# Kernel optimization log

Measured on AMD Instinct MI355X. Metric: run time of the kernel, lower is better.

Reference implementation:

```python
import jax, jax.numpy as jnp
import numpy as np

B, S, E, H, L = 32, 1024, 768, 64, 2  # batch, seq (<=1024 per bias buffer), embed, head hidden, labels
MASKED_BIAS = jnp.float32(-10000.0)


def setup_inputs() -> dict:
    key = jax.random.key(0)
    ks = jax.random.split(key, 12)
    s = 0.02  # init scale
    return {
        "hidden": jax.random.normal(ks[0], (B, S, E), dtype=jnp.float32),
        "attention_mask": jnp.ones((B, S), dtype=jnp.float32),
        # torch nn.Linear weights are [out, in]
        "Wk": jax.random.normal(ks[1], (E, E), dtype=jnp.float32) * s,
        "bk": jnp.zeros((E,), dtype=jnp.float32),
        "Wq": jax.random.normal(ks[2], (E, E), dtype=jnp.float32) * s,
        "bq": jnp.zeros((E,), dtype=jnp.float32),
        "Wv": jax.random.normal(ks[3], (E, E), dtype=jnp.float32) * s,
        "bv": jnp.zeros((E,), dtype=jnp.float32),
        "W1": jax.random.normal(ks[4], (H, E), dtype=jnp.float32) * s,
        "b1": jnp.zeros((H,), dtype=jnp.float32),
        "W2": jax.random.normal(ks[5], (L, H), dtype=jnp.float32) * s,
        "b2": jnp.zeros((L,), dtype=jnp.float32),
    }


def reference(hidden, attention_mask, Wk, bk, Wq, bq, Wv, bv, W1, b1, W2, b2):
    # Single-head causal attention, NO 1/sqrt(d) scaling (faithful to source).
    # Dropout layers run in eval mode -> identity.
    seq = hidden.shape[1]
    q = hidden @ Wq.T + bq            # [B,S,E]
    k = hidden @ Wk.T + bk            # [B,S,E]
    v = hidden @ Wv.T + bv            # [B,S,E] (v_drop is identity in eval)
    w = jnp.einsum('bqe,bke->bqk', q, k)  # [B,S,S]
    causal = jnp.tril(jnp.ones((seq, seq), dtype=bool))  # bias[:, ns-nd:ns, :ns] with nd==ns
    w = jnp.where(causal, w, MASKED_BIAS.astype(w.dtype))
    am = (1.0 - attention_mask)[:, None, :] * -10000.0    # [B,1,S]
    w = jax.nn.softmax(w + am, axis=-1)
    h = jnp.einsum('bqk,bke->bqe', w, v)  # [B,S,E]
    h = jax.nn.relu(h @ W1.T + b1)        # [B,S,64]
    return h @ W2.T + b2                  # [B,S,L]
```

## Files before the change

kernel.cpp:

```cpp
#include <hip/hip_runtime.h>
#include <hip/hip_bf16.h>
#include <cstdio>


typedef _Float16 f16;
typedef f16    f16x8 __attribute__((ext_vector_type(8)));
typedef f16    f16x4 __attribute__((ext_vector_type(4)));
typedef __bf16 bfx8  __attribute__((ext_vector_type(8)));
typedef float  f32x4 __attribute__((ext_vector_type(4)));

#define MFMA_F16(a,b,c)  __builtin_amdgcn_mfma_f32_16x16x32_f16((a),(b),(c),0,0,0)
#define MFMA_BF16(a,b,c) __builtin_amdgcn_mfma_f32_16x16x32_bf16((a),(b),(c),0,0,0)

static constexpr int LDT = 136;
static constexpr int LDT2 = 264;

__device__ __forceinline__ void gl_lds16(const void* g, void* l) {
    __builtin_amdgcn_global_load_lds(
        (const __attribute__((address_space(1))) void*)g,
        (__attribute__((address_space(3))) void*)l, 16, 0, 0);
}

__global__ __launch_bounds__(256) void cvt_f32_f16(
    const float* __restrict__ x, f16* __restrict__ y, int n)
{
    int base = (blockIdx.x * 256 + threadIdx.x) * 4;
    if (base >= n) return;
    f32x4 v = *(const f32x4*)(x + base);
    f16x4 o;
    #pragma unroll
    for (int e = 0; e < 4; ++e) o[e] = (f16)v[e];
    *(f16x4*)(y + base) = o;
}

__global__ __launch_bounds__(256) void cvt3_w(
    const float* __restrict__ Wq, const float* __restrict__ Wk, const float* __restrict__ Wv,
    f16* __restrict__ oq, f16* __restrict__ ok, f16* __restrict__ ov)
{
    const int z = blockIdx.y;
    const float* s = (z == 0) ? Wq : (z == 1) ? Wk : Wv;
    f16* d = (z == 0) ? oq : (z == 1) ? ok : ov;
    int base = (blockIdx.x * 256 + threadIdx.x) * 4;
    f32x4 v = *(const f32x4*)(s + base);
    f16x4 o;
    #pragma unroll
    for (int e = 0; e < 4; ++e) o[e] = (f16)v[e];
    *(f16x4*)(d + base) = o;
}

__global__ __launch_bounds__(1024, 4) void qkv_kernel(
    const f16* __restrict__ h16,
    const f16* __restrict__ wq, const f16* __restrict__ wk, const f16* __restrict__ wv,
    const float* __restrict__ bq, const float* __restrict__ bk, const float* __restrict__ bv,
    f16* __restrict__ q16, f16* __restrict__ k16, __bf16* __restrict__ vT)
{
    const int f = blockIdx.x;
    const int xcd = f & 7;
    const int j = f >> 3;
    const int nt = j % 3;
    const int z  = (j / 3) % 3;
    const int mi = j / 9;
    const int mt = xcd + 8 * mi;
    const int m0 = mt * 256, n0 = nt * 256;

    const f16* W = (z == 0) ? wq : (z == 1) ? wk : wv;
    const float* bias = (z == 0) ? bq : (z == 1) ? bk : bv;

    __shared__ alignas(16) char smem[67584];
    f16 (*S)[16384] = (f16 (*)[16384])smem;
    __bf16* Tb = (__bf16*)smem;

    const int t = threadIdx.x, lane = t & 63, wave = t >> 6;
    const int wm = (wave & 3) * 64, wn = (wave >> 2) * 64;
    const int quad = lane >> 4, l16 = lane & 15;

    const f16* gsrc[2];
    int ldst[2];
    #pragma unroll
    for (int u = 0; u < 2; ++u) {
        int c = wave * 2 + u;
        ldst[u] = c * 512;
        int row = (c < 16) ? (m0 + c * 16 + l16) : (n0 + (c - 16) * 16 + l16);
        const f16* base = (c < 16) ? h16 : W;
        gsrc[u] = base + (size_t)row * 768 + quad * 8;
    }

    f32x4 acc[4][4] = {};
    auto stage = [&](int k0, int buf) {
        #pragma unroll
        for (int u = 0; u < 2; ++u)
            gl_lds16(gsrc[u] + k0, &S[buf][ldst[u]]);
    };
    auto compute = [&](int buf) {
        f16x8 af[4], bg[4];
        #pragma unroll
        for (int i = 0; i < 4; ++i) {
            af[i] = *(const f16x8*)&S[buf][(wm / 16 + i) * 512 + quad * 128 + l16 * 8];
            bg[i] = *(const f16x8*)&S[buf][(16 + wn / 16 + i) * 512 + quad * 128 + l16 * 8];
        }
        #pragma unroll
        for (int i = 0; i < 4; ++i)
            #pragma unroll
            for (int jj = 0; jj < 4; ++jj)
                acc[i][jj] = MFMA_F16(af[i], bg[jj], acc[i][jj]);
    };

    stage(0, 0);
    int cur = 0;
    for (int k0 = 32; k0 < 768; k0 += 32) {
        __syncthreads();
        stage(k0, cur ^ 1);
        compute(cur);
        cur ^= 1;
    }
    __syncthreads();
    compute(cur);

    if (z < 2) {
        f16* out = z ? k16 : q16;
        #pragma unroll
        for (int jj = 0; jj < 4; ++jj) {
            int col = n0 + wn + jj * 16 + l16;
            float bb = bias[col];
            #pragma unroll
            for (int i = 0; i < 4; ++i)
                #pragma unroll
                for (int r = 0; r < 4; ++r) {
                    int row = m0 + wm + i * 16 + quad * 4 + r;
                    out[(size_t)row * 768 + col] = (f16)(acc[i][jj][r] + bb);
                }
        }
    } else {
        const int bofs = (m0 >> 10) * 768;
        const int s0 = m0 & 1023;
        #pragma unroll
        for (int half = 0; half < 2; ++half) {
            __syncthreads();
            if ((wn >> 7) == half) {
                int wnl = wn & 127;
                #pragma unroll
                for (int jj = 0; jj < 4; ++jj) {
                    int el = wnl + jj * 16 + l16;
                    float bb = bias[n0 + half * 128 + el];
                    #pragma unroll
                    for (int i = 0; i < 4; ++i)
                        #pragma unroll
                        for (int r = 0; r < 4; ++r) {
                            int sl = wm + i * 16 + quad * 4 + r;
                            Tb[el * LDT2 + sl] = (__bf16)(acc[i][jj][r] + bb);
                        }
                }
            }
            __syncthreads();
            const int ch = (t & 31) * 8;
            const int rbase = t >> 5;
            #pragma unroll
            for (int p = 0; p < 4; ++p) {
                int r2 = rbase + p * 32;
                bfx8 val = *(const bfx8*)&Tb[r2 * LDT2 + ch];
                *(bfx8*)&vT[(size_t)(bofs + n0 + half * 128 + r2) * 1024 + s0 + ch] = val;
            }
        }
    }
}

__global__ __launch_bounds__(512, 4) void logits_kernel(
    const f16* __restrict__ q16, const f16* __restrict__ k16,
    const float* __restrict__ amask, __bf16* __restrict__ pu, float* __restrict__ psum)
{
    const int f = blockIdx.x;
    const int xcd = f & 7;
    const int j = f >> 3;
    const int b = xcd + 8 * (j / 20);
    const int tile = j % 20;
    const int mt = (tile < 2) ? 0 : (tile < 6) ? 1 : (tile < 12) ? 2 : 3;
    const int nt = tile - ((mt == 0) ? 0 : (mt == 1) ? 2 : (mt == 2) ? 6 : 12);
    const int m0 = mt * 256, n0 = nt * 128;
    const size_t pb = (size_t)b << 20;
    const size_t qb = (size_t)b * 1024 * 768;

    __shared__ alignas(16) f16 S[2][24 * 512];
    __shared__ float rs[2][256];

    const int t = threadIdx.x, lane = t & 63, wave = t >> 6;
    const int wm = (wave & 3) * 64, wn = (wave >> 2) * 64;
    const int quad = lane >> 4, l16 = lane & 15;

    const f16* gsrc[3];
    int ldst[3];
    #pragma unroll
    for (int u = 0; u < 3; ++u) {
        int c = wave * 3 + u;
        ldst[u] = c * 512;
        const f16* base = (c < 16) ? (q16 + qb + (size_t)(m0 + c * 16 + l16) * 768)
                                   : (k16 + qb + (size_t)(n0 + (c - 16) * 16 + l16) * 768);
        gsrc[u] = base + quad * 8;
    }

    f32x4 acc[4][4] = {};
    auto stage = [&](int k0, int buf) {
        #pragma unroll
        for (int u = 0; u < 3; ++u)
            gl_lds16(gsrc[u] + k0, &S[buf][ldst[u]]);
    };
    auto compute = [&](int buf) {
        f16x8 af[4], bg[4];
        #pragma unroll
        for (int i = 0; i < 4; ++i) {
            af[i] = *(const f16x8*)&S[buf][(wm / 16 + i) * 512 + quad * 128 + l16 * 8];
            bg[i] = *(const f16x8*)&S[buf][(16 + wn / 16 + i) * 512 + quad * 128 + l16 * 8];
        }
        #pragma unroll
        for (int i = 0; i < 4; ++i)
            #pragma unroll
            for (int jj = 0; jj < 4; ++jj)
                acc[i][jj] = MFMA_F16(af[i], bg[jj], acc[i][jj]);
    };

    stage(0, 0);
    int cur = 0;
    for (int k0 = 32; k0 < 768; k0 += 32) {
        __syncthreads();
        stage(k0, cur ^ 1);
        compute(cur);
        cur ^= 1;
    }
    __syncthreads();
    compute(cur);

    float rp[4][4] = {};
    #pragma unroll
    for (int jj = 0; jj < 4; ++jj) {
        int col = n0 + wn + jj * 16 + l16;
        float am = (1.0f - amask[b * 1024 + col]) * -10000.0f;
        #pragma unroll
        for (int i = 0; i < 4; ++i)
            #pragma unroll
            for (int r = 0; r < 4; ++r) {
                int row = m0 + wm + i * 16 + quad * 4 + r;
                float s = acc[i][jj][r] + am;
                float pval = (col <= row) ? __expf(fminf(s, 80.0f)) : 0.0f;
                pu[pb + (size_t)row * 1024 + col] = (__bf16)pval;
                rp[i][r] += pval;
            }
    }
    #pragma unroll
    for (int i = 0; i < 4; ++i)
        #pragma unroll
        for (int r = 0; r < 4; ++r) {
            float v = rp[i][r];
            v += __shfl_xor(v, 1, 64);
            v += __shfl_xor(v, 2, 64);
            v += __shfl_xor(v, 4, 64);
            v += __shfl_xor(v, 8, 64);
            if (l16 == 0) rs[wn >> 6][wm + i * 16 + quad * 4 + r] = v;
        }
    __syncthreads();
    if (t < 256)
        psum[((size_t)b * 1024 + m0 + t) * 8 + nt] = rs[0][t] + rs[1][t];
}

__global__ __launch_bounds__(512, 4) void pv_kernel(
    const __bf16* __restrict__ pu, const __bf16* __restrict__ vT,
    const float* __restrict__ psum, __bf16* __restrict__ h)
{
    const int f = blockIdx.x;
    const int xcd = f & 7;
    const int j = f >> 3;
    const int b = xcd + 8 * (j / 24);
    const int tile = j % 24;
    const int mt = tile / 6, nt = tile % 6;
    const int m0 = mt * 256, n0 = nt * 128;
    const size_t pb = (size_t)b << 20;
    const size_t vb = (size_t)b * 768 * 1024;

    __shared__ alignas(16) __bf16 S[2][24 * 512];
    __shared__ float invl[256];

    const int t = threadIdx.x, lane = t & 63, wave = t >> 6;
    const int wm = (wave & 3) * 64, wn = (wave >> 2) * 64;
    const int quad = lane >> 4, l16 = lane & 15;

    if (t < 256) {
        int row = m0 + t;
        int lim = row >> 7;
        const float* pr = &psum[((size_t)b * 1024 + row) * 8];
        float s = 0.f;
        #pragma unroll
        for (int n = 0; n < 8; ++n) s += (n <= lim) ? pr[n] : 0.f;
        invl[t] = 1.0f / s;
    }

    const __bf16* gsrc[3];
    int ldst[3];
    #pragma unroll
    for (int u = 0; u < 3; ++u) {
        int c = wave * 3 + u;
        ldst[u] = c * 512;
        const __bf16* base = (c < 16) ? (pu + pb + (size_t)(m0 + c * 16 + l16) * 1024)
                                      : (vT + vb + (size_t)(n0 + (c - 16) * 16 + l16) * 1024);
        gsrc[u] = base + quad * 8;
    }

    f32x4 acc[4][4] = {};
    auto stage = [&](int k0, int buf) {
        #pragma unroll
        for (int u = 0; u < 3; ++u)
            gl_lds16(gsrc[u] + k0, &S[buf][ldst[u]]);
    };
    auto compute = [&](int buf) {
        bfx8 af[4], bg[4];
        #pragma unroll
        for (int i = 0; i < 4; ++i) {
            af[i] = *(const bfx8*)&S[buf][(wm / 16 + i) * 512 + quad * 128 + l16 * 8];
            bg[i] = *(const bfx8*)&S[buf][(16 + wn / 16 + i) * 512 + quad * 128 + l16 * 8];
        }
        #pragma unroll
        for (int i = 0; i < 4; ++i)
            #pragma unroll
            for (int jj = 0; jj < 4; ++jj)
                acc[i][jj] = MFMA_BF16(af[i], bg[jj], acc[i][jj]);
    };

    const int kend = m0 + 256;
    stage(0, 0);
    int cur = 0;
    for (int k0 = 32; k0 < kend; k0 += 32) {
        __syncthreads();
        stage(k0, cur ^ 1);
        compute(cur);
        cur ^= 1;
    }
    __syncthreads();
    compute(cur);

    #pragma unroll
    for (int jj = 0; jj < 4; ++jj) {
        int col = n0 + wn + jj * 16 + l16;
        #pragma unroll
        for (int i = 0; i < 4; ++i)
            #pragma unroll
            for (int r = 0; r < 4; ++r) {
                int rl = wm + i * 16 + quad * 4 + r;
                h[((size_t)b * 1024 + m0 + rl) * 768 + col] = (__bf16)(acc[i][jj][r] * invl[rl]);
            }
    }
}

__global__ __launch_bounds__(256) void mlp_kernel(
    const __bf16* __restrict__ h, const float* __restrict__ W1, const float* __restrict__ b1,
    const float* __restrict__ W2, const float* __restrict__ b2, float* __restrict__ out)
{
    const int wave = threadIdx.x >> 6, lane = threadIdx.x & 63;
    const int quad = lane >> 4, l16 = lane & 15;
    const int m0 = blockIdx.x * 64 + wave * 16;

    f32x4 acc[4] = {};
    for (int k0 = 0; k0 < 768; k0 += 32) {
        bfx8 af = *(const bfx8*)&h[(size_t)(m0 + l16) * 768 + k0 + quad * 8];
        #pragma unroll
        for (int jj = 0; jj < 4; ++jj) {
            const float* wp = W1 + (size_t)(jj * 16 + l16) * 768 + k0 + quad * 8;
            f32x4 w0 = *(const f32x4*)wp;
            f32x4 w1 = *(const f32x4*)(wp + 4);
            bfx8 bg;
            #pragma unroll
            for (int e = 0; e < 4; ++e) { bg[e] = (__bf16)w0[e]; bg[e + 4] = (__bf16)w1[e]; }
            acc[jj] = MFMA_BF16(af, bg, acc[jj]);
        }
    }
    float part[4][2] = {};
    #pragma unroll
    for (int jj = 0; jj < 4; ++jj) {
        int c = jj * 16 + l16;
        float bb = b1[c];
        float w20 = W2[c], w21 = W2[64 + c];
        #pragma unroll
        for (int r = 0; r < 4; ++r) {
            float x = fmaxf(acc[jj][r] + bb, 0.f);
            part[r][0] += x * w20;
            part[r][1] += x * w21;
        }
    }
    #pragma unroll
    for (int off = 1; off < 16; off <<= 1)
        #pragma unroll
        for (int r = 0; r < 4; ++r) {
            part[r][0] += __shfl_xor(part[r][0], off, 64);
            part[r][1] += __shfl_xor(part[r][1], off, 64);
        }
    if (l16 == 0) {
        #pragma unroll
        for (int r = 0; r < 4; ++r) {
            int row = m0 + quad * 4 + r;
            out[(size_t)row * 2 + 0] = part[r][0] + b2[0];
            out[(size_t)row * 2 + 1] = part[r][1] + b2[1];
        }
    }
}

extern "C" void kernel_launch(void* const* d_in, const int* in_sizes, int n_in,
                              void* d_out, int out_size, void* d_ws, size_t ws_size,
                              hipStream_t stream)
{
    const float* hidden = (const float*)d_in[0];
    const float* amask  = (const float*)d_in[1];
    const float* Wk = (const float*)d_in[2];
    const float* bk = (const float*)d_in[3];
    const float* Wq = (const float*)d_in[4];
    const float* bq = (const float*)d_in[5];
    const float* Wv = (const float*)d_in[6];
    const float* bv = (const float*)d_in[7];
    const float* W1 = (const float*)d_in[8];
    const float* b1 = (const float*)d_in[9];
    const float* W2 = (const float*)d_in[10];
    const float* b2 = (const float*)d_in[11];
    float* out = (float*)d_out;

    char* ws = (char*)d_ws;
    const size_t MB = 1024 * 1024;
    f16* h16 = (f16*)ws;
    f16* wq16 = (f16*)(ws + 48 * MB);
    f16* wk16 = wq16 + 589824;
    f16* wv16 = wk16 + 589824;
    __bf16* pu  = (__bf16*)ws;
    float*  psum = (float*)(ws + 64 * MB);
    f16* q16 = (f16*)(ws + 66 * MB);
    f16* k16 = (f16*)(ws + 114 * MB);
    __bf16* vT = (__bf16*)(ws + 162 * MB);
    __bf16* h  = (__bf16*)(ws + 66 * MB);
    const size_t NEED = 210 * MB;
    if (ws_size < NEED) {
        fprintf(stderr, "[Attn kernel] ws too small: %zu < %zu — skipping launches\n",
                ws_size, NEED);
        return;
    }

    cvt_f32_f16<<<24576, 256, 0, stream>>>(hidden, h16, 25165824);
    cvt3_w<<<dim3(576, 3), 256, 0, stream>>>(Wq, Wk, Wv, wq16, wk16, wv16);

    qkv_kernel<<<1152, 1024, 0, stream>>>(
        h16, wq16, wk16, wv16, bq, bk, bv, q16, k16, vT);
    logits_kernel<<<640, 512, 0, stream>>>(q16, k16, amask, pu, psum);
    pv_kernel<<<768, 512, 0, stream>>>(pu, vT, psum, h);
    mlp_kernel<<<512, 256, 0, stream>>>(h, W1, b1, W2, b2, out);
}
```

Measured before the change: 548.6 us.

## Enlarge logits and PV tiles to 256x256 with 1024-thread blocks; fuse convert kernels

Result: no change. 538.2 us (-1.9%).

```diff
diff --git a/kernel.cpp b/kernel.cpp
--- a/kernel.cpp
+++ b/kernel.cpp
@@ -12,7 +12,6 @@
 #define MFMA_F16(a,b,c)  __builtin_amdgcn_mfma_f32_16x16x32_f16((a),(b),(c),0,0,0)
 #define MFMA_BF16(a,b,c) __builtin_amdgcn_mfma_f32_16x16x32_bf16((a),(b),(c),0,0,0)
 
-static constexpr int LDT = 136;
 static constexpr int LDT2 = 264;
 
 __device__ __forceinline__ void gl_lds16(const void* g, void* l) {
@@ -21,31 +20,29 @@
         (__attribute__((address_space(3))) void*)l, 16, 0, 0);
 }
 
-__global__ __launch_bounds__(256) void cvt_f32_f16(
-    const float* __restrict__ x, f16* __restrict__ y, int n)
-{
-    int base = (blockIdx.x * 256 + threadIdx.x) * 4;
-    if (base >= n) return;
-    f32x4 v = *(const f32x4*)(x + base);
+__global__ __launch_bounds__(256) void cvt_all(
+    const float* __restrict__ hidden,
+    const float* __restrict__ Wq, const float* __restrict__ Wk, const float* __restrict__ Wv,
+    f16* __restrict__ h16, f16* __restrict__ oq, f16* __restrict__ ok, f16* __restrict__ ov)
+{
+    const int bid = blockIdx.x;
+    const float* src;
+    f16* dst;
+    int base;
+    if (bid < 24576) {
+        src = hidden; dst = h16;
+        base = (bid * 256 + threadIdx.x) * 4;
+    } else {
+        int wz = (bid - 24576) / 576, wb = (bid - 24576) % 576;
+        src = (wz == 0) ? Wq : (wz == 1) ? Wk : Wv;
+        dst = (wz == 0) ? oq : (wz == 1) ? ok : ov;
+        base = (wb * 256 + threadIdx.x) * 4;
+    }
+    f32x4 v = *(const f32x4*)(src + base);
     f16x4 o;
     #pragma unroll
     for (int e = 0; e < 4; ++e) o[e] = (f16)v[e];
-    *(f16x4*)(y + base) = o;
-}
-
-__global__ __launch_bounds__(256) void cvt3_w(
-    const float* __restrict__ Wq, const float* __restrict__ Wk, const float* __restrict__ Wv,
-    f16* __restrict__ oq, f16* __restrict__ ok, f16* __restrict__ ov)
-{
-    const int z = blockIdx.y;
-    const float* s = (z == 0) ? Wq : (z == 1) ? Wk : Wv;
-    f16* d = (z == 0) ? oq : (z == 1) ? ok : ov;
-    int base = (blockIdx.x * 256 + threadIdx.x) * 4;
-    f32x4 v = *(const f32x4*)(s + base);
-    f16x4 o;
-    #pragma unroll
-    for (int e = 0; e < 4; ++e) o[e] = (f16)v[e];
-    *(f16x4*)(d + base) = o;
+    *(f16x4*)(dst + base) = o;
 }
 
 __global__ __launch_bounds__(1024, 4) void qkv_kernel(
@@ -164,33 +161,36 @@
     }
 }
 
-__global__ __launch_bounds__(512, 4) void logits_kernel(
+__global__ __launch_bounds__(1024, 4) void logits_kernel(
     const f16* __restrict__ q16, const f16* __restrict__ k16,
     const float* __restrict__ amask, __bf16* __restrict__ pu, float* __restrict__ psum)
 {
     const int f = blockIdx.x;
     const int xcd = f & 7;
     const int j = f >> 3;
-    const int b = xcd + 8 * (j / 20);
-    const int tile = j % 20;
-    const int mt = (tile < 2) ? 0 : (tile < 6) ? 1 : (tile < 12) ? 2 : 3;
-    const int nt = tile - ((mt == 0) ? 0 : (mt == 1) ? 2 : (mt == 2) ? 6 : 12);
-    const int m0 = mt * 256, n0 = nt * 128;
+    const int b = xcd + 8 * (j / 10);
+    const int tile = j % 10;
+    int mt, nt;
+    if (tile < 4)      { mt = 3; nt = tile; }
+    else if (tile < 7) { mt = 2; nt = tile - 4; }
+    else if (tile < 9) { mt = 1; nt = tile - 7; }
+    else               { mt = 0; nt = 0; }
+    const int m0 = mt * 256, n0 = nt * 256;
     const size_t pb = (size_t)b << 20;
     const size_t qb = (size_t)b * 1024 * 768;
 
-    __shared__ alignas(16) f16 S[2][24 * 512];
-    __shared__ float rs[2][256];
+    __shared__ alignas(16) f16 S[2][32 * 512];
+    __shared__ float rs[4][256];
 
     const int t = threadIdx.x, lane = t & 63, wave = t >> 6;
     const int wm = (wave & 3) * 64, wn = (wave >> 2) * 64;
     const int quad = lane >> 4, l16 = lane & 15;
 
-    const f16* gsrc[3];
-    int ldst[3];
-    #pragma unroll
-    for (int u = 0; u < 3; ++u) {
-        int c = wave * 3 + u;
+    const f16* gsrc[2];
+    int ldst[2];
+    #pragma unroll
+    for (int u = 0; u < 2; ++u) {
+        int c = wave * 2 + u;
         ldst[u] = c * 512;
         const f16* base = (c < 16) ? (q16 + qb + (size_t)(m0 + c * 16 + l16) * 768)
                                    : (k16 + qb + (size_t)(n0 + (c - 16) * 16 + l16) * 768);
@@ -200,7 +200,7 @@
     f32x4 acc[4][4] = {};
     auto stage = [&](int k0, int buf) {
         #pragma unroll
-        for (int u = 0; u < 3; ++u)
+        for (int u = 0; u < 2; ++u)
             gl_lds16(gsrc[u] + k0, &S[buf][ldst[u]]);
     };
     auto compute = [&](int buf) {
@@ -257,24 +257,25 @@
         }
     __syncthreads();
     if (t < 256)
-        psum[((size_t)b * 1024 + m0 + t) * 8 + nt] = rs[0][t] + rs[1][t];
-}
-
-__global__ __launch_bounds__(512, 4) void pv_kernel(
+        psum[((size_t)b * 1024 + m0 + t) * 4 + nt] =
+            rs[0][t] + rs[1][t] + rs[2][t] + rs[3][t];
+}
+
+__global__ __launch_bounds__(1024, 4) void pv_kernel(
     const __bf16* __restrict__ pu, const __bf16* __restrict__ vT,
     const float* __restrict__ psum, __bf16* __restrict__ h)
 {
     const int f = blockIdx.x;
     const int xcd = f & 7;
     const int j = f >> 3;
-    const int b = xcd + 8 * (j / 24);
-    const int tile = j % 24;
-    const int mt = tile / 6, nt = tile % 6;
-    const int m0 = mt * 256, n0 = nt * 128;
+    const int b = xcd + 8 * (j / 12);
+    const int tile = j % 12;
+    const int mt = 3 - tile / 3, nt = tile % 3;
+    const int m0 = mt * 256, n0 = nt * 256;
     const size_t pb = (size_t)b << 20;
     const size_t vb = (size_t)b * 768 * 1024;
 
-    __shared__ alignas(16) __bf16 S[2][24 * 512];
+    __shared__ alignas(16) __bf16 S[2][32 * 512];
     __shared__ float invl[256];
 
     const int t = threadIdx.x, lane = t & 63, wave = t >> 6;
@@ -283,19 +284,19 @@
 
     if (t < 256) {
         int row = m0 + t;
-        int lim = row >> 7;
-        const float* pr = &psum[((size_t)b * 1024 + row) * 8];
+        int lim = row >> 8;
+        const float* pr = &psum[((size_t)b * 1024 + row) * 4];
         float s = 0.f;
         #pragma unroll
-        for (int n = 0; n < 8; ++n) s += (n <= lim) ? pr[n] : 0.f;
+        for (int n = 0; n < 4; ++n) s += (n <= lim) ? pr[n] : 0.f;
         invl[t] = 1.0f / s;
     }
 
-    const __bf16* gsrc[3];
-    int ldst[3];
-    #pragma unroll
-    for (int u = 0; u < 3; ++u) {
-        int c = wave * 3 + u;
+    const __bf16* gsrc[2];
+    int ldst[2];
+    #pragma unroll
+    for (int u = 0; u < 2; ++u) {
+        int c = wave * 2 + u;
         ldst[u] = c * 512;
         const __bf16* base = (c < 16) ? (pu + pb + (size_t)(m0 + c * 16 + l16) * 1024)
                                       : (vT + vb + (size_t)(n0 + (c - 16) * 16 + l16) * 1024);
@@ -305,7 +306,7 @@
     f32x4 acc[4][4] = {};
     auto stage = [&](int k0, int buf) {
         #pragma unroll
-        for (int u = 0; u < 3; ++u)
+        for (int u = 0; u < 2; ++u)
             gl_lds16(gsrc[u] + k0, &S[buf][ldst[u]]);
     };
     auto compute = [&](int buf) {
@@ -436,12 +437,12 @@
         return;
     }
 
-    cvt_f32_f16<<<24576, 256, 0, stream>>>(hidden, h16, 25165824);
-    cvt3_w<<<dim3(576, 3), 256, 0, stream>>>(Wq, Wk, Wv, wq16, wk16, wv16);
+    cvt_all<<<24576 + 1728, 256, 0, stream>>>(
+        hidden, Wq, Wk, Wv, h16, wq16, wk16, wv16);
 
     qkv_kernel<<<1152, 1024, 0, stream>>>(
         h16, wq16, wk16, wv16, bq, bk, bv, q16, k16, vT);
-    logits_kernel<<<640, 512, 0, stream>>>(q16, k16, amask, pu, psum);
-    pv_kernel<<<768, 512, 0, stream>>>(pu, vT, psum, h);
+    logits_kernel<<<320, 1024, 0, stream>>>(q16, k16, amask, pu, psum);
+    pv_kernel<<<384, 1024, 0, stream>>>(pu, vT, psum, h);
     mlp_kernel<<<512, 256, 0, stream>>>(h, W1, b1, W2, b2, out);
 }
```
